# Kernel tuning notes

Hardware: AMD Instinct MI355X
Metric: run time of the kernel (lower is better)

The kernel has to match this reference:

```python
import jax, jax.numpy as jnp
import numpy as np

B, C, H, W = 16, 256, 32, 32
K = 3          # kernel size
KK = K * K     # matrix_batch = 9 kernel positions
N = 256        # out_channels = n (power of 2, nstack = 1)


def setup_inputs() -> dict:
    key = jax.random.key(0)
    k1, k2, k3, k4 = jax.random.split(key, 4)
    s = 1.0 / np.sqrt(2.0)  # repo's 'regular' param init scale
    return {
        "x": jax.random.normal(k1, (B, C, H, W), jnp.float32),
        "twiddle1": jax.random.normal(k2, (KK, N - 1, 2, 2), jnp.float32) * s,
        "twiddle2": jax.random.normal(k3, (KK, N - 1, 2, 2), jnp.float32) * s,
        "bias": jax.random.normal(k4, (KK, N), jnp.float32) * 0.01,
    }


def _butterfly_tied(twiddle, x, increasing):
    """Tied-weight butterfly multiply.
    twiddle: (s, n-1, 2, 2); x: (b, s, n). At stride st, twiddle[:, st-1:2*st-1]
    (length st) is shared across the n/(2*st) blocks (matches butterfly_mult_torch).
    """
    b, s, n = x.shape
    m = n.bit_length() - 1  # log2(n)
    strides = [1 << i for i in range(m)]
    if not increasing:
        strides = strides[::-1]
    for st in strides:
        t = twiddle[:, st - 1:2 * st - 1]            # (s, st, 2, 2)
        xr = x.reshape(b, s, n // (2 * st), 2, st)   # (b, s, g, 2, st)
        # out[b,s,g,i,l] = sum_k t[s,l,i,k] * xr[b,s,g,k,l]
        x = jnp.einsum('slik,bsgkl->bsgil', t, xr).reshape(b, s, n)
    return x


def reference(x, twiddle1, twiddle2, bias):
    b, c, h, w = x.shape
    # im2col / F.unfold with kernel 3, pad 1, stride 1 -> (b, c, 9, h*w),
    # kernel positions in row-major order (matches torch unfold layout).
    xp = jnp.pad(x, ((0, 0), (0, 0), (1, 1), (1, 1)))
    patches = jnp.stack(
        [xp[:, :, i:i + h, j:j + w] for i in range(K) for j in range(K)], axis=2
    )  # (b, c, 9, h, w)
    inp = patches.reshape(b, c, KK, h * w).transpose(0, 3, 2, 1)
    inp = inp.reshape(b * h * w, KK, c)  # (batch*h*w, 9, c)
    # BB^T: B^T (decreasing stride) then B (increasing stride), bias on last.
    y = _butterfly_tied(twiddle1, inp, increasing=False)
    y = _butterfly_tied(twiddle2, y, increasing=True) + bias  # bias: (9, N)
    out = y.mean(axis=1)  # average over the 9 kernel positions -> (b*h*w, N)
    return out.reshape(b, h * w, N).transpose(0, 2, 1).reshape(b, N, h, w)
```

## Files before the change

### kernel.cpp

```cpp
#include <hip/hip_runtime.h>
#include <hip/hip_bf16.h>

typedef __attribute__((ext_vector_type(8))) short short8;
typedef __attribute__((ext_vector_type(16))) float float16v;

#define XT_BYTES (16*32*34*34*8*2)
#define WG_BYTES (9*4*4*8*64*8*2)

__global__ __launch_bounds__(256) void k_transpose(const float* __restrict__ x,
                                                   __hip_bfloat16* __restrict__ xTg) {
  __shared__ float tile[256 * 33];
  char* xTB = (char*)xTg;
  int blk = blockIdx.x;
  int h = blk & 31, b = blk >> 5;
  int tid = threadIdx.x;
  {
    int w4 = (tid & 7) * 4, c0 = tid >> 3;
#pragma unroll
    for (int j = 0; j < 8; ++j) {
      int ci = c0 + 32 * j;
      float4 v = *(const float4*)&x[((b * 256 + ci) * 32 + h) * 32 + w4];
      *(float4*)&tile[ci * 33 + w4] = v;
    }
  }
  __syncthreads();
  {
    int g0 = tid >> 5, w = tid & 31;
#pragma unroll
    for (int gi = 0; gi < 4; ++gi) {
      int g = gi * 8 + g0;
      union { short8 s; __hip_bfloat16 hv[8]; } pk;
#pragma unroll
      for (int cc = 0; cc < 8; ++cc)
        pk.hv[cc] = __float2bfloat16(tile[(g * 8 + cc) * 33 + w]);
      *(short8*)(xTB + ((((b * 32 + g) * 34 + h + 1) * 34) + (w + 1)) * 16) = pk.s;
    }
  }
  if (h < 2) {
    uint4 z4 = {0u, 0u, 0u, 0u};
    int edge = h * 33;
    for (int i = tid; i < 32 * 34; i += 256) {
      int g = i / 34, w = i - g * 34;
      *(uint4*)(xTB + ((((b * 32 + g) * 34 + edge) * 34) + w) * 16) = z4;
    }
    for (int i = tid; i < 32 * 32; i += 256) {
      int g = i >> 5, hh = 1 + (i & 31);
      *(uint4*)(xTB + ((((b * 32 + g) * 34 + hh) * 34) + edge) * 16) = z4;
    }
  }
}

__global__ __launch_bounds__(256) void k_build_w(const float* __restrict__ tw1,
                                                 const float* __restrict__ tw2,
                                                 const float* __restrict__ bias,
                                                 __hip_bfloat16* __restrict__ Wg,
                                                 float* __restrict__ biasout) {
  __shared__ float mat[256 * 17];
  __shared__ __align__(16) float tws[2 * 255 * 4];
  int blk = blockIdx.x;
  int tid = threadIdx.x;
  if (blk == 144) {
    if (tid < 256) {
      float a = 0.f;
#pragma unroll
      for (int s = 0; s < 9; ++s) a += bias[s * 256 + tid];
      biasout[tid] = a * (1.f / 9.f);
    }
    return;
  }
  int sidx = blk >> 4;
  int colbase = (blk & 15) * 16;

  for (int i = tid; i < 255 * 4; i += 256) {
    tws[i]           = tw1[sidx * 255 * 4 + i];
    tws[255 * 4 + i] = tw2[sidx * 255 * 4 + i];
  }
  {
    int r = tid;
#pragma unroll
    for (int c = 0; c < 16; ++c) mat[r * 17 + c] = (r == colbase + c) ? 1.f : 0.f;
  }

  int c  = tid & 15;
  int pg = tid >> 4;
  for (int ph = 0; ph < 2; ++ph) {
    for (int si = 0; si < 8; ++si) {
      int lg = ph ? si : (7 - si);
      int st = 1 << lg;
      __syncthreads();
      float x0[8], x1[8], t0[8], t1[8], t2[8], t3[8];
#pragma unroll
      for (int i = 0; i < 8; ++i) {
        int qp = pg * 8 + i;
        int li = qp & (st - 1);
        int gi = qp >> lg;
        int p0 = (gi << (lg + 1)) | li;
        int p1 = p0 + st;
        float4 tv = *(const float4*)&tws[(ph * 255 + st - 1 + li) * 4];
        t0[i] = tv.x; t1[i] = tv.y; t2[i] = tv.z; t3[i] = tv.w;
        x0[i] = mat[p0 * 17 + c];
        x1[i] = mat[p1 * 17 + c];
      }
#pragma unroll
      for (int i = 0; i < 8; ++i) {
        int qp = pg * 8 + i;
        int li = qp & (st - 1);
        int gi = qp >> lg;
        int p0 = (gi << (lg + 1)) | li;
        int p1 = p0 + st;
        mat[p0 * 17 + c] = t0[i] * x0[i] + t1[i] * x1[i];
        mat[p1 * 17 + c] = t2[i] * x0[i] + t3[i] * x1[i];
      }
    }
  }
  __syncthreads();

  for (int idx = tid; idx < 256 * 16; idx += 256) {
    int r = idx >> 4, cc = idx & 15;
    int cg = colbase + cc;
    int pr = cg >> 6, g = (cg >> 3) & 7, c8 = cg & 7;
    int nq = r >> 6, nl = r & 63;
    int o = ((((sidx * 4 + pr) * 4 + nq) * 8 + g) * 64 + nl) * 8 + c8;
    Wg[o] = __float2bfloat16(mat[r * 17 + cc] * (1.f / 9.f));
  }
}

#define ABUF 8192

__global__ __launch_bounds__(256, 4) void k_gemm(const __hip_bfloat16* __restrict__ xTg,
                                                 const __hip_bfloat16* __restrict__ Wg,
                                                 const float* __restrict__ biasout,
                                                 float* __restrict__ out) {
  __shared__ __align__(64) char lds[2 * ABUF];
  const char* WgB = (const char*)Wg;
  const char* xTB = (const char*)xTg;

  int blk = blockIdx.x;
  int nq = blk & 3;
  int pt = (blk >> 2) & 15;
  int b  = blk >> 6;
  int h0 = pt * 2;

  int tid  = threadIdx.x;
  int lane = tid & 63;
  int wk   = tid >> 6;
  int half = lane >> 5;
  int l31  = lane & 31;

  float16v acc[2][2];
#pragma unroll
  for (int mt = 0; mt < 2; ++mt)
#pragma unroll
    for (int p2 = 0; p2 < 2; ++p2)
#pragma unroll
      for (int e = 0; e < 16; ++e) acc[mt][p2][e] = 0.f;

  int aoff[2];
#pragma unroll
  for (int mt = 0; mt < 2; ++mt)
    aoff[mt] = ((2 * wk + half) * 64 + mt * 32 + l31) * 16;

  int bbase = ((b * 32 + 2 * wk + half) * 34 + h0) * 34 + l31;

  auto stage_a = [&](int step, int buf) {
    int p = step / 9, s = step - p * 9;
    const char* g = WgB + ((s * 4 + p) * 4 + nq) * 8192;
#pragma unroll
    for (int i = 0; i < 2; ++i) {
      int slotbase = i * 256 + wk * 64;
      __builtin_amdgcn_global_load_lds(
          (const __attribute__((address_space(1))) void*)(g + (slotbase + lane) * 16),
          (__attribute__((address_space(3))) void*)(lds + buf * ABUF + slotbase * 16),
          16, 0, 0);
    }
  };

  auto load_b = [&](int step, short8* bf) {
    int p = step / 9, s = step - p * 9;
    int si = s / 3, sj = s - si * 3;
    int off = (bbase + p * (8 * 34 * 34) + si * 34 + sj) * 16;
    bf[0] = *(const short8*)(xTB + off);
    bf[1] = *(const short8*)(xTB + off + 34 * 16);
  };

  short8 bcur[2], bnext[2];
  stage_a(0, 0);
  load_b(0, bcur);
  __syncthreads();

  for (int step = 0; step < 36; ++step) {
    if (step < 35) {
      stage_a(step + 1, (step + 1) & 1);
      load_b(step + 1, bnext);
    }
    int abase = (step & 1) * ABUF;
    short8 af0 = *(const short8*)(lds + abase + aoff[0]);
    short8 af1 = *(const short8*)(lds + abase + aoff[1]);
    acc[0][0] = __builtin_amdgcn_mfma_f32_32x32x16_bf16(af0, bcur[0], acc[0][0], 0, 0, 0);
    acc[0][1] = __builtin_amdgcn_mfma_f32_32x32x16_bf16(af0, bcur[1], acc[0][1], 0, 0, 0);
    acc[1][0] = __builtin_amdgcn_mfma_f32_32x32x16_bf16(af1, bcur[0], acc[1][0], 0, 0, 0);
    acc[1][1] = __builtin_amdgcn_mfma_f32_32x32x16_bf16(af1, bcur[1], acc[1][1], 0, 0, 0);
    __syncthreads();
    bcur[0] = bnext[0];
    bcur[1] = bnext[1];
  }

  auto fptr = [&](int slot) { return (float16v*)(lds + slot * 4096 + lane * 64); };
  __syncthreads();
  if (wk >= 2) { *fptr((wk - 2) * 2 + 0) = acc[0][0]; *fptr((wk - 2) * 2 + 1) = acc[0][1]; }
  __syncthreads();
  if (wk < 2)  { acc[0][0] += *fptr(wk * 2 + 0); acc[0][1] += *fptr(wk * 2 + 1); }
  __syncthreads();
  if (wk >= 2) { *fptr((wk - 2) * 2 + 0) = acc[1][0]; *fptr((wk - 2) * 2 + 1) = acc[1][1]; }
  __syncthreads();
  if (wk < 2)  { acc[1][0] += *fptr(wk * 2 + 0); acc[1][1] += *fptr(wk * 2 + 1); }
  __syncthreads();
  if (wk == 1) { *fptr(0) = acc[0][0]; *fptr(1) = acc[0][1];
                 *fptr(2) = acc[1][0]; *fptr(3) = acc[1][1]; }
  __syncthreads();
  if (wk == 0) {
    acc[0][0] += *fptr(0); acc[0][1] += *fptr(1);
    acc[1][0] += *fptr(2); acc[1][1] += *fptr(3);
#pragma unroll
    for (int mt = 0; mt < 2; ++mt) {
#pragma unroll
      for (int reg = 0; reg < 16; ++reg) {
        int n = nq * 64 + mt * 32 + (reg & 3) + 8 * (reg >> 2) + 4 * half;
        float bv = biasout[n];
        out[((b * 256 + n) * 32 + h0) * 32 + l31]     = acc[mt][0][reg] + bv;
        out[((b * 256 + n) * 32 + h0 + 1) * 32 + l31] = acc[mt][1][reg] + bv;
      }
    }
  }
}

extern "C" void kernel_launch(void* const* d_in, const int* in_sizes, int n_in,
                              void* d_out, int out_size, void* d_ws, size_t ws_size,
                              hipStream_t stream) {
  const float* x    = (const float*)d_in[0];
  const float* tw1  = (const float*)d_in[1];
  const float* tw2  = (const float*)d_in[2];
  const float* bias = (const float*)d_in[3];
  float* out = (float*)d_out;

  char* ws = (char*)d_ws;
  __hip_bfloat16* xTg = (__hip_bfloat16*)ws;
  __hip_bfloat16* Wg  = (__hip_bfloat16*)(ws + XT_BYTES);
  float* biasout      = (float*)(ws + XT_BYTES + WG_BYTES);

  k_transpose<<<512, 256, 0, stream>>>(x, xTg);
  k_build_w<<<145, 256, 0, stream>>>(tw1, tw2, bias, Wg, biasout);
  k_gemm<<<1024, 256, 0, stream>>>(xTg, Wg, biasout, out);
}
```

Before: 119.0 us.

## Merge prep kernels and load GEMM A operands directly from global

Fuses the input transpose and butterfly-weight build kernels into one launch, with the block index selecting the role, so one kernel launch and its gap are removed. In the GEMM, the LDS double-buffered A staging with a per-step barrier is replaced by direct per-lane global loads of A and B inside a fully unrolled 3x3 inner loop, so the main loop no longer synchronises. The trade-off is that the A tile is re-read from global/L2 by each wave instead of being shared through LDS, and prefetching now depends on the compiler's scheduling.

```diff
diff --git a/kernel.cpp b/kernel.cpp
--- a/kernel.cpp
+++ b/kernel.cpp
@@ -7,59 +7,60 @@
 #define XT_BYTES (16*32*34*34*8*2)
 #define WG_BYTES (9*4*4*8*64*8*2)
 
-__global__ __launch_bounds__(256) void k_transpose(const float* __restrict__ x,
-                                                   __hip_bfloat16* __restrict__ xTg) {
-  __shared__ float tile[256 * 33];
-  char* xTB = (char*)xTg;
-  int blk = blockIdx.x;
-  int h = blk & 31, b = blk >> 5;
-  int tid = threadIdx.x;
-  {
-    int w4 = (tid & 7) * 4, c0 = tid >> 3;
-#pragma unroll
-    for (int j = 0; j < 8; ++j) {
-      int ci = c0 + 32 * j;
-      float4 v = *(const float4*)&x[((b * 256 + ci) * 32 + h) * 32 + w4];
-      *(float4*)&tile[ci * 33 + w4] = v;
-    }
-  }
-  __syncthreads();
-  {
-    int g0 = tid >> 5, w = tid & 31;
-#pragma unroll
-    for (int gi = 0; gi < 4; ++gi) {
-      int g = gi * 8 + g0;
-      union { short8 s; __hip_bfloat16 hv[8]; } pk;
-#pragma unroll
-      for (int cc = 0; cc < 8; ++cc)
-        pk.hv[cc] = __float2bfloat16(tile[(g * 8 + cc) * 33 + w]);
-      *(short8*)(xTB + ((((b * 32 + g) * 34 + h + 1) * 34) + (w + 1)) * 16) = pk.s;
-    }
-  }
-  if (h < 2) {
-    uint4 z4 = {0u, 0u, 0u, 0u};
-    int edge = h * 33;
-    for (int i = tid; i < 32 * 34; i += 256) {
-      int g = i / 34, w = i - g * 34;
-      *(uint4*)(xTB + ((((b * 32 + g) * 34 + edge) * 34) + w) * 16) = z4;
-    }
-    for (int i = tid; i < 32 * 32; i += 256) {
-      int g = i >> 5, hh = 1 + (i & 31);
-      *(uint4*)(xTB + ((((b * 32 + g) * 34 + hh) * 34) + edge) * 16) = z4;
-    }
-  }
-}
-
-__global__ __launch_bounds__(256) void k_build_w(const float* __restrict__ tw1,
-                                                 const float* __restrict__ tw2,
-                                                 const float* __restrict__ bias,
-                                                 __hip_bfloat16* __restrict__ Wg,
-                                                 float* __restrict__ biasout) {
-  __shared__ float mat[256 * 17];
-  __shared__ __align__(16) float tws[2 * 255 * 4];
+__global__ __launch_bounds__(256) void k_prep(const float* __restrict__ x,
+                                              const float* __restrict__ tw1,
+                                              const float* __restrict__ tw2,
+                                              const float* __restrict__ bias,
+                                              __hip_bfloat16* __restrict__ xTg,
+                                              __hip_bfloat16* __restrict__ Wg,
+                                              float* __restrict__ biasout) {
+  __shared__ __align__(16) char smem[256 * 33 * 4];
   int blk = blockIdx.x;
   int tid = threadIdx.x;
-  if (blk == 144) {
+
+  if (blk < 512) {
+    float* tile = (float*)smem;
+    char* xTB = (char*)xTg;
+    int h = blk & 31, b = blk >> 5;
+    {
+      int w4 = (tid & 7) * 4, c0 = tid >> 3;
+#pragma unroll
+      for (int j = 0; j < 8; ++j) {
+        int ci = c0 + 32 * j;
+        float4 v = *(const float4*)&x[((b * 256 + ci) * 32 + h) * 32 + w4];
+        *(float4*)&tile[ci * 33 + w4] = v;
+      }
+    }
+    __syncthreads();
+    {
+      int g0 = tid >> 5, w = tid & 31;
+#pragma unroll
+      for (int gi = 0; gi < 4; ++gi) {
+        int g = gi * 8 + g0;
+        union { short8 s; __hip_bfloat16 hv[8]; } pk;
+#pragma unroll
+        for (int cc = 0; cc < 8; ++cc)
+          pk.hv[cc] = __float2bfloat16(tile[(g * 8 + cc) * 33 + w]);
+        *(short8*)(xTB + ((((b * 32 + g) * 34 + h + 1) * 34) + (w + 1)) * 16) = pk.s;
+      }
+    }
+    if (h < 2) {
+      uint4 z4 = {0u, 0u, 0u, 0u};
+      int edge = h * 33;
+      for (int i = tid; i < 32 * 34; i += 256) {
+        int g = i / 34, w = i - g * 34;
+        *(uint4*)(xTB + ((((b * 32 + g) * 34 + edge) * 34) + w) * 16) = z4;
+      }
+      for (int i = tid; i < 32 * 32; i += 256) {
+        int g = i >> 5, hh = 1 + (i & 31);
+        *(uint4*)(xTB + ((((b * 32 + g) * 34 + hh) * 34) + edge) * 16) = z4;
+      }
+    }
+    return;
+  }
+
+  int wblk = blk - 512;
+  if (wblk == 144) {
     if (tid < 256) {
       float a = 0.f;
 #pragma unroll
@@ -68,8 +69,10 @@
     }
     return;
   }
-  int sidx = blk >> 4;
-  int colbase = (blk & 15) * 16;
+  float* mat = (float*)smem;
+  float* tws = (float*)(smem + 17408);
+  int sidx = wblk >> 4;
+  int colbase = (wblk & 15) * 16;
 
   for (int i = tid; i < 255 * 4; i += 256) {
     tws[i]           = tw1[sidx * 255 * 4 + i];
@@ -125,13 +128,11 @@
   }
 }
 
-#define ABUF 8192
-
 __global__ __launch_bounds__(256, 4) void k_gemm(const __hip_bfloat16* __restrict__ xTg,
                                                  const __hip_bfloat16* __restrict__ Wg,
                                                  const float* __restrict__ biasout,
                                                  float* __restrict__ out) {
-  __shared__ __align__(64) char lds[2 * ABUF];
+  __shared__ __align__(64) char lds[16384];
   const char* WgB = (const char*)Wg;
   const char* xTB = (const char*)xTg;
 
@@ -155,54 +156,27 @@
 #pragma unroll
       for (int e = 0; e < 16; ++e) acc[mt][p2][e] = 0.f;
 
-  int aoff[2];
-#pragma unroll
-  for (int mt = 0; mt < 2; ++mt)
-    aoff[mt] = ((2 * wk + half) * 64 + mt * 32 + l31) * 16;
-
-  int bbase = ((b * 32 + 2 * wk + half) * 34 + h0) * 34 + l31;
-
-  auto stage_a = [&](int step, int buf) {
-    int p = step / 9, s = step - p * 9;
-    const char* g = WgB + ((s * 4 + p) * 4 + nq) * 8192;
-#pragma unroll
-    for (int i = 0; i < 2; ++i) {
-      int slotbase = i * 256 + wk * 64;
-      __builtin_amdgcn_global_load_lds(
-          (const __attribute__((address_space(1))) void*)(g + (slotbase + lane) * 16),
-          (__attribute__((address_space(3))) void*)(lds + buf * ABUF + slotbase * 16),
-          16, 0, 0);
-    }
-  };
-
-  auto load_b = [&](int step, short8* bf) {
-    int p = step / 9, s = step - p * 9;
-    int si = s / 3, sj = s - si * 3;
-    int off = (bbase + p * (8 * 34 * 34) + si * 34 + sj) * 16;
-    bf[0] = *(const short8*)(xTB + off);
-    bf[1] = *(const short8*)(xTB + off + 34 * 16);
-  };
-
-  short8 bcur[2], bnext[2];
-  stage_a(0, 0);
-  load_b(0, bcur);
-  __syncthreads();
-
-  for (int step = 0; step < 36; ++step) {
-    if (step < 35) {
-      stage_a(step + 1, (step + 1) & 1);
-      load_b(step + 1, bnext);
-    }
-    int abase = (step & 1) * ABUF;
-    short8 af0 = *(const short8*)(lds + abase + aoff[0]);
-    short8 af1 = *(const short8*)(lds + abase + aoff[1]);
-    acc[0][0] = __builtin_amdgcn_mfma_f32_32x32x16_bf16(af0, bcur[0], acc[0][0], 0, 0, 0);
-    acc[0][1] = __builtin_amdgcn_mfma_f32_32x32x16_bf16(af0, bcur[1], acc[0][1], 0, 0, 0);
-    acc[1][0] = __builtin_amdgcn_mfma_f32_32x32x16_bf16(af1, bcur[0], acc[1][0], 0, 0, 0);
-    acc[1][1] = __builtin_amdgcn_mfma_f32_32x32x16_bf16(af1, bcur[1], acc[1][1], 0, 0, 0);
-    __syncthreads();
-    bcur[0] = bnext[0];
-    bcur[1] = bnext[1];
+  int aoff = ((2 * wk + half) * 64 + l31) * 16;
+  int bbase = ((((b * 32 + 2 * wk + half) * 34 + h0) * 34) + l31) * 16;
+
+  for (int p = 0; p < 4; ++p) {
+    const char* Bp = xTB + bbase + p * (8 * 34 * 34) * 16;
+    const char* Ap = WgB + (p * 4 + nq) * 8192;
+    for (int si = 0; si < 3; ++si) {
+#pragma unroll
+      for (int sj = 0; sj < 3; ++sj) {
+        const char* Aslab = Ap + (si * 3 + sj) * (16 * 8192);
+        short8 a0 = *(const short8*)(Aslab + aoff);
+        short8 a1 = *(const short8*)(Aslab + aoff + 32 * 16);
+        const char* Bq = Bp + (si * 34 + sj) * 16;
+        short8 b0 = *(const short8*)(Bq);
+        short8 b1 = *(const short8*)(Bq + 34 * 16);
+        acc[0][0] = __builtin_amdgcn_mfma_f32_32x32x16_bf16(a0, b0, acc[0][0], 0, 0, 0);
+        acc[0][1] = __builtin_amdgcn_mfma_f32_32x32x16_bf16(a0, b1, acc[0][1], 0, 0, 0);
+        acc[1][0] = __builtin_amdgcn_mfma_f32_32x32x16_bf16(a1, b0, acc[1][0], 0, 0, 0);
+        acc[1][1] = __builtin_amdgcn_mfma_f32_32x32x16_bf16(a1, b1, acc[1][1], 0, 0, 0);
+      }
+    }
   }
 
   auto fptr = [&](int slot) { return (float16v*)(lds + slot * 4096 + lane * 64); };
@@ -248,7 +222,6 @@
   __hip_bfloat16* Wg  = (__hip_bfloat16*)(ws + XT_BYTES);
   float* biasout      = (float*)(ws + XT_BYTES + WG_BYTES);
 
-  k_transpose<<<512, 256, 0, stream>>>(x, xTg);
-  k_build_w<<<145, 256, 0, stream>>>(tw1, tw2, bias, Wg, biasout);
+  k_prep<<<657, 256, 0, stream>>>(x, tw1, tw2, bias, xTg, Wg, biasout);
   k_gemm<<<1024, 256, 0, stream>>>(xTg, Wg, biasout, out);
 }
```

New measurement: 111.9 us. 1.06x faster.
